# Kernel optimization log

Measured on AMD Instinct MI355X. Metric: run time of the kernel, lower is better.

The kernel has to match this reference:

```python
import jax, jax.numpy as jnp
import numpy as np

VOL = (256, 256, 256)
K = 64  # number of connected components (clusters)


def setup_inputs() -> dict:
    key = jax.random.key(0)
    k1, k2, k3 = jax.random.split(key, 3)
    # Precomputed connected-component labels of (pred + target) > 0.
    # 0 = background, 1..K = clusters.
    labels = jax.random.randint(k1, VOL, 0, K + 1, dtype=jnp.int32)
    fg = labels > 0
    # Binary prediction / ground-truth masks, nonzero only inside labeled regions
    # (consistent with labels being components of the overlay of pred and target).
    pred = ((jax.random.uniform(k2, VOL) < 0.6) & fg).astype(jnp.float32)
    target = ((jax.random.uniform(k3, VOL) < 0.6) & fg).astype(jnp.float32)
    return {"pred": pred, "target": target, "labels": labels, "num_clusters": K}


def reference(pred, target, labels, num_clusters):
    # Per-cluster dice via one fused segment reduction instead of a Python loop
    # over clusters. Segment 0 is background and is dropped, matching
    # range(1, num_features + 1) in the original.
    lab = labels.reshape(-1)
    p = pred.reshape(-1)
    t = target.reshape(-1)
    nseg = num_clusters + 1
    # intersection = sum(pred_cluster * gt_cluster); pred/target are binary so
    # logical_and(...).float() products reduce to pred * target per segment.
    inter = jax.ops.segment_sum(p * t, lab, num_segments=nseg)[1:]
    sum_p = jax.ops.segment_sum(p, lab, num_segments=nseg)[1:]
    sum_t = jax.ops.segment_sum(t, lab, num_segments=nseg)[1:]
    union = sum_p + sum_t
    dice = jnp.where(union > 0, 2.0 * inter / jnp.maximum(union, 1.0), 1.0)
    return 1.0 - jnp.mean(dice)
```

## Files before the change

kernel.cpp:

```cpp
#include <hip/hip_runtime.h>


#define NBIN 65
#define NREP 64
#define REP_MASK 63
#define BLOCKS 1024
#define THREADS 256

typedef float4 f4;
typedef int4 i4;

#define GLOAD(dst, voff, base) \
    asm volatile("global_load_dwordx4 %0, %1, %2" \
                 : "=v"(dst) : "v"(voff), "s"(base))

#define WAITN(NSTR) do { \
    asm volatile("s_waitcnt vmcnt(" NSTR ")" ::: "memory"); \
    __builtin_amdgcn_sched_barrier(0); \
} while (0)

#define ISSUE(X) do { \
    GLOAD(P##X##0, vo0, pred);   GLOAD(P##X##1, vo1, pred); \
    GLOAD(P##X##2, vo2, pred);   GLOAD(P##X##3, vo3, pred); \
    GLOAD(T##X##0, vo0, target); GLOAD(T##X##1, vo1, target); \
    GLOAD(T##X##2, vo2, target); GLOAD(T##X##3, vo3, target); \
    GLOAD(L##X##0, vo0, labels); GLOAD(L##X##1, vo1, labels); \
    GLOAD(L##X##2, vo2, labels); GLOAD(L##X##3, vo3, labels); \
} while (0)

#define ADV() do { vo0 += 16384u; vo1 += 16384u; vo2 += 16384u; vo3 += 16384u; } while (0)

#define PROCESS(X) do { \
    rmw_group(hist, tid, P##X##0, T##X##0, L##X##0); \
    rmw_group(hist, tid, P##X##1, T##X##1, L##X##1); \
    rmw_group(hist, tid, P##X##2, T##X##2, L##X##2); \
    rmw_group(hist, tid, P##X##3, T##X##3, L##X##3); \
} while (0)

__device__ __forceinline__ unsigned int contrib(float p, float t) {
    unsigned int sp = (p != 0.0f) ? 1u : 0u;
    unsigned int st = (t != 0.0f) ? 1u : 0u;
    return ((sp & st) << 8) | (sp + st);
}

__device__ __forceinline__ void rmw_group(unsigned short* hist, int tid,
                                          f4 p, f4 t, i4 l) {
    const int i0 = l.x * THREADS + tid;
    const int i1 = l.y * THREADS + tid;
    const int i2 = l.z * THREADS + tid;
    const int i3 = l.w * THREADS + tid;
    const unsigned int d0 = hist[i0];
    const unsigned int d1 = hist[i1];
    const unsigned int d2 = hist[i2];
    const unsigned int d3 = hist[i3];
    const unsigned int c0 = contrib(p.x, t.x);
    const unsigned int c1 = contrib(p.y, t.y);
    const unsigned int c2 = contrib(p.z, t.z);
    const unsigned int c3 = contrib(p.w, t.w);
    const unsigned int e0 = c0;
    const unsigned int e1 = c1 + ((i1 == i0) ? e0 : 0u);
    const unsigned int e2 = c2 + ((i2 == i1) ? e1 : ((i2 == i0) ? e0 : 0u));
    const unsigned int e3 = c3 + ((i3 == i2) ? e2 :
                             ((i3 == i1) ? e1 : ((i3 == i0) ? e0 : 0u)));
    hist[i0] = (unsigned short)(d0 + e0);
    hist[i1] = (unsigned short)(d1 + e1);
    hist[i2] = (unsigned short)(d2 + e2);
    hist[i3] = (unsigned short)(d3 + e3);
}

__global__ __launch_bounds__(THREADS, 3) void seg_count_kernel(
    const float* __restrict__ pred,
    const float* __restrict__ target,
    const int* __restrict__ labels,
    unsigned long long* __restrict__ part,
    int n)
{
    __shared__ unsigned short s_hist[NBIN][THREADS];
    const int tid = threadIdx.x;
    const int rep = (int)blockIdx.x & REP_MASK;
    unsigned short* hist = &s_hist[0][0];

    unsigned int* hz = (unsigned int*)s_hist;
    for (int i = tid; i < NBIN * THREADS / 2; i += THREADS) hz[i] = 0u;
    __syncthreads();

    const int n_vec = n >> 2;
    const int chunk = (n_vec + (int)gridDim.x - 1) / (int)gridDim.x;
    const int base = blockIdx.x * chunk;
    const int end = min(base + chunk, n_vec);

    if (end - base == 16 * THREADS) {
        f4 PA0, PA1, PA2, PA3, TA0, TA1, TA2, TA3;
        f4 PB0, PB1, PB2, PB3, TB0, TB1, TB2, TB3;
        i4 LA0, LA1, LA2, LA3, LB0, LB1, LB2, LB3;
        unsigned int vo0 = (unsigned int)(base + tid) * 16u;
        unsigned int vo1 = vo0 + 4096u;
        unsigned int vo2 = vo0 + 8192u;
        unsigned int vo3 = vo0 + 12288u;

        ISSUE(A);
        ADV();
        ISSUE(B);
        WAITN("12");
        PROCESS(A);
        ADV();
        ISSUE(A);
        WAITN("12");
        PROCESS(B);
        ADV();
        ISSUE(B);
        WAITN("12");
        PROCESS(A);
        WAITN("0");
        PROCESS(B);
    } else {
        const f4* __restrict__ p4 = (const f4*)pred;
        const f4* __restrict__ t4 = (const f4*)target;
        const i4* __restrict__ l4 = (const i4*)labels;
        for (int idx = base + tid; idx < end; idx += THREADS)
            rmw_group(hist, tid, p4[idx], t4[idx], l4[idx]);
    }

    if (blockIdx.x == 0) {
        for (int i = (n_vec << 2) + tid; i < n; i += THREADS)
            hist[labels[i] * THREADS + tid] =
                (unsigned short)(hist[labels[i] * THREADS + tid] +
                                 contrib(pred[i], target[i]));
    }
    __syncthreads();

    const int s = 1 + (tid >> 2);
    const int q = tid & 3;
    const unsigned long long* row =
        (const unsigned long long*)&s_hist[s][q * 64];
    unsigned long long accU = 0, accI = 0;
    const int rot = tid & 15;
    #pragma unroll
    for (int j = 0; j < 16; ++j) {
        int i = (j + rot) & 15;
        unsigned long long v = row[i];
        accU += v & 0x00FF00FF00FF00FFull;
        accI += (v >> 8) & 0x00FF00FF00FF00FFull;
    }
    accU += accU >> 32;
    accI += accI >> 32;
    unsigned int U = ((unsigned int)accU & 0xFFFFu) + (((unsigned int)accU >> 16) & 0xFFFFu);
    unsigned int I = ((unsigned int)accI & 0xFFFFu) + (((unsigned int)accI >> 16) & 0xFFFFu);

    U += __shfl_xor(U, 1); U += __shfl_xor(U, 2);
    I += __shfl_xor(I, 1); I += __shfl_xor(I, 2);
    if (q == 0) {
        unsigned long long tot =
            ((unsigned long long)I << 32) | (unsigned long long)U;
        if (tot) atomicAdd(&part[(s - 1) * NREP + rep], tot);
    }
}

__global__ __launch_bounds__(256) void dice_finalize_kernel(
    const unsigned long long* __restrict__ part,
    const int* __restrict__ nc_ptr,
    float* __restrict__ out)
{
    const int nc = *nc_ptr;
    const int tid = threadIdx.x;
    const int s = 1 + (tid >> 2);
    const int q = tid & 3;

    unsigned long long acc = 0;
    const unsigned long long* row = part + (s - 1) * NREP + q * 16;
    #pragma unroll
    for (int i = 0; i < 16; ++i) acc += row[i];
    acc += __shfl_xor(acc, 1);
    acc += __shfl_xor(acc, 2);

    __shared__ float s_dice[64];
    if (q == 0) {
        float U = (float)(unsigned int)(acc & 0xFFFFFFFFull);
        float I = (float)(unsigned int)(acc >> 32);
        float dice = (U > 0.0f) ? (2.0f * I / U) : 1.0f;
        s_dice[s - 1] = (s <= nc) ? dice : 0.0f;
    }
    __syncthreads();

    if (tid < 64) {
        float local = s_dice[tid];
        #pragma unroll
        for (int off = 32; off > 0; off >>= 1)
            local += __shfl_down(local, off);
        if (tid == 0) out[0] = 1.0f - local / (float)nc;
    }
}

extern "C" void kernel_launch(void* const* d_in, const int* in_sizes, int n_in,
                              void* d_out, int out_size, void* d_ws, size_t ws_size,
                              hipStream_t stream) {
    const float* pred   = (const float*)d_in[0];
    const float* target = (const float*)d_in[1];
    const int*   labels = (const int*)d_in[2];
    const int*   nc_ptr = (const int*)d_in[3];
    float* out = (float*)d_out;
    unsigned long long* part = (unsigned long long*)d_ws;

    const int n = in_sizes[0];

    hipMemsetAsync(d_ws, 0, 64 * NREP * sizeof(unsigned long long), stream);

    seg_count_kernel<<<BLOCKS, THREADS, 0, stream>>>(
        pred, target, labels, part, n);
    dice_finalize_kernel<<<1, 256, 0, stream>>>(part, nc_ptr, out);
}
```

Baseline: 202.9 us.

## Replace 12-deep load batches with 2-slot rolling pipeline and raise occupancy

The fast path now keeps two in-flight groups of three dwordx4 loads (pred, target, labels) instead of two batches of twelve, processing one 16-byte group while the next is in flight. The 16 groups each block handles are walked starting at a block-dependent rotation offset, which staggers the address streams across blocks. Fewer live vector registers allow launch bounds to request 4 blocks per SIMD instead of 3, trading per-wave memory-level parallelism for more resident waves.

```diff
diff --git a/kernel.cpp b/kernel.cpp
--- a/kernel.cpp
+++ b/kernel.cpp
@@ -19,23 +19,12 @@
     __builtin_amdgcn_sched_barrier(0); \
 } while (0)
 
-#define ISSUE(X) do { \
-    GLOAD(P##X##0, vo0, pred);   GLOAD(P##X##1, vo1, pred); \
-    GLOAD(P##X##2, vo2, pred);   GLOAD(P##X##3, vo3, pred); \
-    GLOAD(T##X##0, vo0, target); GLOAD(T##X##1, vo1, target); \
-    GLOAD(T##X##2, vo2, target); GLOAD(T##X##3, vo3, target); \
-    GLOAD(L##X##0, vo0, labels); GLOAD(L##X##1, vo1, labels); \
-    GLOAD(L##X##2, vo2, labels); GLOAD(L##X##3, vo3, labels); \
+#define ISSUE1(X, g) do { \
+    unsigned int vo = vbase + (((unsigned int)(g)) & 15u) * 4096u; \
+    GLOAD(P##X, vo, pred); GLOAD(T##X, vo, target); GLOAD(L##X, vo, labels); \
 } while (0)
 
-#define ADV() do { vo0 += 16384u; vo1 += 16384u; vo2 += 16384u; vo3 += 16384u; } while (0)
-
-#define PROCESS(X) do { \
-    rmw_group(hist, tid, P##X##0, T##X##0, L##X##0); \
-    rmw_group(hist, tid, P##X##1, T##X##1, L##X##1); \
-    rmw_group(hist, tid, P##X##2, T##X##2, L##X##2); \
-    rmw_group(hist, tid, P##X##3, T##X##3, L##X##3); \
-} while (0)
+#define PROC(X) rmw_group(hist, tid, P##X, T##X, L##X)
 
 __device__ __forceinline__ unsigned int contrib(float p, float t) {
     unsigned int sp = (p != 0.0f) ? 1u : 0u;
@@ -68,7 +57,7 @@
     hist[i3] = (unsigned short)(d3 + e3);
 }
 
-__global__ __launch_bounds__(THREADS, 3) void seg_count_kernel(
+__global__ __launch_bounds__(THREADS, 4) void seg_count_kernel(
     const float* __restrict__ pred,
     const float* __restrict__ target,
     const int* __restrict__ labels,
@@ -90,29 +79,22 @@
     const int end = min(base + chunk, n_vec);
 
     if (end - base == 16 * THREADS) {
-        f4 PA0, PA1, PA2, PA3, TA0, TA1, TA2, TA3;
-        f4 PB0, PB1, PB2, PB3, TB0, TB1, TB2, TB3;
-        i4 LA0, LA1, LA2, LA3, LB0, LB1, LB2, LB3;
-        unsigned int vo0 = (unsigned int)(base + tid) * 16u;
-        unsigned int vo1 = vo0 + 4096u;
-        unsigned int vo2 = vo0 + 8192u;
-        unsigned int vo3 = vo0 + 12288u;
+        const int g0 = ((int)blockIdx.x >> 3) & 15;
+        const unsigned int vbase = (unsigned int)(base + tid) * 16u;
+        f4 PA, TA, PB, TB;
+        i4 LA, LB;
 
-        ISSUE(A);
-        ADV();
-        ISSUE(B);
-        WAITN("12");
-        PROCESS(A);
-        ADV();
-        ISSUE(A);
-        WAITN("12");
-        PROCESS(B);
-        ADV();
-        ISSUE(B);
-        WAITN("12");
-        PROCESS(A);
-        WAITN("0");
-        PROCESS(B);
+        ISSUE1(A, g0);
+        ISSUE1(B, g0 + 1);
+        #pragma unroll
+        for (int j = 0; j < 16; j += 2) {
+            WAITN("3");
+            PROC(A);
+            if (j + 2 < 16) ISSUE1(A, g0 + j + 2);
+            if (j + 3 < 16) { WAITN("3"); } else { WAITN("0"); }
+            PROC(B);
+            if (j + 3 < 16) ISSUE1(B, g0 + j + 3);
+        }
     } else {
         const f4* __restrict__ p4 = (const f4*)pred;
         const f4* __restrict__ t4 = (const f4*)target;
```

Result: no change. 206.1 us (+1.6%).
